# Kernel tuning notes

Hardware: AMD Instinct MI355X
Metric: run time of the kernel (lower is better)

The kernel has to match this reference:

```python
import jax, jax.numpy as jnp
import numpy as np

DIM = 1024
NUM_HEADS = 16
HEAD_DIM = DIM // NUM_HEADS


def setup_inputs() -> dict:
    key = jax.random.key(0)
    ks = jax.random.split(key, 9)
    s = 1.0 / np.sqrt(DIM)
    x = jax.random.normal(ks[0], (2, 2048, DIM), dtype=jnp.float32)
    Wq = jax.random.uniform(ks[1], (DIM, DIM), jnp.float32, -s, s)
    bq = jax.random.uniform(ks[2], (DIM,), jnp.float32, -s, s)
    Wk = jax.random.uniform(ks[3], (DIM, DIM), jnp.float32, -s, s)
    bk = jax.random.uniform(ks[4], (DIM,), jnp.float32, -s, s)
    Wv = jax.random.uniform(ks[5], (DIM, DIM), jnp.float32, -s, s)
    bv = jax.random.uniform(ks[6], (DIM,), jnp.float32, -s, s)
    Wo = jax.random.uniform(ks[7], (DIM, DIM), jnp.float32, -s, s)
    bo = jax.random.uniform(ks[8], (DIM,), jnp.float32, -s, s)
    return {"x": x, "Wq": Wq, "bq": bq, "Wk": Wk, "bk": bk,
            "Wv": Wv, "bv": bv, "Wo": Wo, "bo": bo}


def reference(x, Wq, bq, Wk, bk, Wv, bv, Wo, bo):
    B, S, _ = x.shape
    # projections (torch Linear: y = x @ W.T + b); split heads -> [B, H, S, Dh]
    def split(y):
        return y.reshape(B, S, NUM_HEADS, HEAD_DIM).transpose(0, 2, 1, 3)
    q = split(x @ Wq.T + bq)
    k = split(x @ Wk.T + bk)
    v = split(x @ Wv.T + bv)
    scale = 1.0 / np.sqrt(HEAD_DIM).astype(np.float32)
    scores = jnp.einsum('bhqd,bhkd->bhqk', q, k) * scale  # [B,H,S,S]
    attn = jax.nn.softmax(scores, axis=-1)
    ctx = jnp.einsum('bhqk,bhkd->bhqd', attn, v)  # [B,H,S,Dh]
    ctx = ctx.transpose(0, 2, 1, 3).reshape(B, S, DIM)
    return ctx @ Wo.T + bo
```

## Files before the change

kernel.cpp:

```cpp
#include <hip/hip_runtime.h>
#include <hip/hip_bf16.h>
#include <math.h>

#define DIMSZ 1024
#define NHEAD 16
#define HDIM 64
#define BATCH 2
#define SEQ 2048
#define NROWS (BATCH * SEQ)

#define QSCALE 0.18033688011112042592f

typedef __attribute__((ext_vector_type(8))) _Float16 f16x8;
typedef __attribute__((ext_vector_type(2))) __fp16 fp16x2;
typedef __attribute__((ext_vector_type(4))) float f32x4;

__device__ __forceinline__ ushort f2h(float x) {
    union { _Float16 h; ushort u; } cv;
    cv.h = (_Float16)x;
    return cv.u;
}

__device__ __forceinline__ unsigned pkrtz(float a, float b) {
    union { fp16x2 v; unsigned u; } c;
    c.v = __builtin_amdgcn_cvt_pkrtz(a, b);
    return c.u;
}

__device__ __forceinline__ void gld16(const void* g, void* l) {
    __builtin_amdgcn_global_load_lds((const __attribute__((address_space(1))) void*)g,
                                     (__attribute__((address_space(3))) void*)l,
                                     16, 0, 0);
}

__global__ __launch_bounds__(256) void convert_all(
    const float* __restrict__ x,
    const float* __restrict__ Wq, const float* __restrict__ Wk,
    const float* __restrict__ Wv, const float* __restrict__ Wo,
    ushort* __restrict__ Xh, ushort* __restrict__ Wh, ushort* __restrict__ Woh)
{
    const int b = blockIdx.x;
    const float* src;
    ushort* dst;
    size_t off;
    if (b < 2048)      { src = x;  dst = Xh;             off = (size_t)b * 2048; }
    else if (b < 2560) { src = Wq; dst = Wh;             off = (size_t)(b - 2048) * 2048; }
    else if (b < 3072) { src = Wk; dst = Wh + (1 << 20); off = (size_t)(b - 2560) * 2048; }
    else if (b < 3584) { src = Wv; dst = Wh + 2 * (1 << 20); off = (size_t)(b - 3072) * 2048; }
    else               { src = Wo; dst = Woh;            off = (size_t)(b - 3584) * 2048; }

    const size_t i = off + (size_t)threadIdx.x * 8;
    const float4 f0 = *(const float4*)&src[i];
    const float4 f1 = *(const float4*)&src[i + 4];
    uint4 hv;
    hv.x = (unsigned)f2h(f0.x) | ((unsigned)f2h(f0.y) << 16);
    hv.y = (unsigned)f2h(f0.z) | ((unsigned)f2h(f0.w) << 16);
    hv.z = (unsigned)f2h(f1.x) | ((unsigned)f2h(f1.y) << 16);
    hv.w = (unsigned)f2h(f1.z) | ((unsigned)f2h(f1.w) << 16);
    *(uint4*)&dst[i] = hv;
}

__global__ __launch_bounds__(256, 3) void qkv_gemm(
    const ushort* __restrict__ Xh,
    const ushort* __restrict__ Wh,
    const float* __restrict__ bq, const float* __restrict__ bk,
    const float* __restrict__ bv,
    ushort* __restrict__ Qb, ushort* __restrict__ Kb, ushort* __restrict__ Vt)
{
    __shared__ __align__(16) ushort smem[17408];

    const int tid = threadIdx.x;
    const int wave = tid >> 6;
    const int lane = tid & 63;
    const int lm = lane & 15;
    const int lq = lane >> 4;
    const int wy = wave >> 1;
    const int wx = wave & 1;
    const int m0 = blockIdx.x * 128;
    const int nbase = blockIdx.y * 128;

    const int c = tid & 7;
    const int r0 = tid >> 3;
    const int g = c ^ (r0 & 7);
    const ushort* gah = Xh + (size_t)(m0 + r0) * DIMSZ + g * 8;
    const ushort* gbh = Wh + (size_t)(nbase + r0) * DIMSZ + g * 8;
    const int tofs = tid * 8;

    int aofs[4][2], bofs[4][2];
#pragma unroll
    for (int i = 0; i < 4; ++i)
#pragma unroll
        for (int kt = 0; kt < 2; ++kt) {
            const int slot = ((kt * 4 + lq) ^ (lm & 7)) << 3;
            aofs[i][kt] = (wy * 64 + i * 16 + lm) * 64 + slot;
            bofs[i][kt] = 8192 + (wx * 64 + i * 16 + lm) * 64 + slot;
        }

    f32x4 acc[4][4] = {};

#pragma unroll
    for (int gg = 0; gg < 4; ++gg) {
        gld16(gah + gg * 32 * DIMSZ, smem + gg * 2048 + tofs);
        gld16(gbh + gg * 32 * DIMSZ, smem + 8192 + gg * 2048 + tofs);
    }

    for (int kk = 0; kk < 16; ++kk) {
        __syncthreads();

        f16x8 a0[4], b0[4];
#pragma unroll
        for (int i = 0; i < 4; ++i) {
            a0[i] = *(const f16x8*)&smem[aofs[i][0]];
            b0[i] = *(const f16x8*)&smem[bofs[i][0]];
        }
#pragma unroll
        for (int i = 0; i < 4; ++i)
#pragma unroll
            for (int j = 0; j < 4; ++j)
                acc[i][j] = __builtin_amdgcn_mfma_f32_16x16x32_f16(a0[i], b0[j], acc[i][j], 0, 0, 0);

        f16x8 a1[4], b1[4];
#pragma unroll
        for (int i = 0; i < 4; ++i) {
            a1[i] = *(const f16x8*)&smem[aofs[i][1]];
            b1[i] = *(const f16x8*)&smem[bofs[i][1]];
        }

        __syncthreads();

        if (kk + 1 < 16) {
            const int k0 = (kk + 1) * 64;
#pragma unroll
            for (int gg = 0; gg < 4; ++gg) {
                gld16(gah + gg * 32 * DIMSZ + k0, smem + gg * 2048 + tofs);
                gld16(gbh + gg * 32 * DIMSZ + k0, smem + 8192 + gg * 2048 + tofs);
            }
        }

#pragma unroll
        for (int i = 0; i < 4; ++i)
#pragma unroll
            for (int j = 0; j < 4; ++j)
                acc[i][j] = __builtin_amdgcn_mfma_f32_16x16x32_f16(a1[i], b1[j], acc[i][j], 0, 0, 0);
    }

    const int mat = blockIdx.y >> 3;
    const float* bias = (mat == 0) ? bq : (mat == 1) ? bk : bv;
    const int nloc0 = (blockIdx.y & 7) * 128;
    const int b = m0 >> 11;
    const int s0 = m0 & (SEQ - 1);
    ushort* sf = smem;

    __syncthreads();

    if (mat == 2) {
#pragma unroll
        for (int j = 0; j < 4; ++j) {
            const int nc = nloc0 + wx * 64 + j * 16 + lm;
            const float bb = bias[nc];
            const int d = j * 16 + lm;
#pragma unroll
            for (int i = 0; i < 4; ++i) {
                const int ss = wy * 64 + (i >> 1) * 32 + lq * 8 + (i & 1) * 4;
                ushort4 pk;
                pk.x = f2h(acc[i][j][0] + bb);
                pk.y = f2h(acc[i][j][1] + bb);
                pk.z = f2h(acc[i][j][2] + bb);
                pk.w = f2h(acc[i][j][3] + bb);
                *(ushort4*)&sf[(wx * 64 + d) * 136 + ss] = pk;
            }
        }
        __syncthreads();
#pragma unroll
        for (int p = 0; p < 8; ++p) {
            const int idx = p * 256 + tid;
            const int row = idx >> 4;
            const int hh = row >> 6;
            const int d = row & 63;
            const int sseg = (idx & 15) * 8;
            const uint4 v = *(const uint4*)&sf[row * 136 + sseg];
            const int hg = (nloc0 >> 6) + hh;
            *(uint4*)&Vt[((size_t)(b * NHEAD + hg) * HDIM + d) * SEQ + s0 + sseg] = v;
        }
    } else {
        ushort* dst = (mat == 0) ? Qb : Kb;
        const float sc = (mat == 0) ? QSCALE : 1.0f;
#pragma unroll
        for (int j = 0; j < 4; ++j) {
            const int col = wx * 64 + j * 16 + lm;
            const float bb = bias[nloc0 + col];
#pragma unroll
            for (int i = 0; i < 4; ++i) {
                const int rbase = wy * 64 + i * 16 + lq * 4;
#pragma unroll
                for (int rr = 0; rr < 4; ++rr)
                    sf[(rbase + rr) * 136 + col] = f2h((acc[i][j][rr] + bb) * sc);
            }
        }
        __syncthreads();
#pragma unroll
        for (int p = 0; p < 8; ++p) {
            const int idx = p * 256 + tid;
            const int row = idx >> 4;
            const int seg = idx & 15;
            const uint4 v = *(const uint4*)&sf[row * 136 + seg * 8];
            const int nc0 = nloc0 + seg * 8;
            const int h = nc0 >> 6;
            const int d = nc0 & 63;
            *(uint4*)&dst[((size_t)(b * NHEAD + h) * SEQ + s0 + row) * HDIM + d] = v;
        }
    }
}

__global__ __launch_bounds__(256, 2) void flash_attn_mfma(
    const ushort* __restrict__ Qb, const ushort* __restrict__ Kb,
    const ushort* __restrict__ Vt, ushort* __restrict__ CTXh)
{
    __shared__ __align__(16) ushort Ks[2][8192];
    __shared__ __align__(16) ushort Vs[2][8192];

    const int tid = threadIdx.x;
    const int w = tid >> 6;
    const int l = tid & 63;
    const int lm = l & 15;
    const int lq = l >> 4;
    const int q0 = blockIdx.x * 128;
    const int bh = blockIdx.y;
    const int NCH = SEQ / 128;

    const int ch0 = (bh >> 4) * 8;

    const ushort* Kg = Kb + (size_t)bh * SEQ * HDIM;
    const ushort* Vg = Vt + (size_t)bh * HDIM * SEQ;

    const int sr8 = l >> 3;
    const int sg_ = (l & 7) ^ (sr8 & 7);

    f16x8 qf[2][2];
#pragma unroll
    for (int rt = 0; rt < 2; ++rt)
#pragma unroll
        for (int kt = 0; kt < 2; ++kt)
            qf[rt][kt] = *(const f16x8*)&Qb[((size_t)bh * SEQ + q0 + w * 32 + rt * 16 + lm) * HDIM + kt * 32 + lq * 8];

    int kbase[2], vbase[4];
#pragma unroll
    for (int kt = 0; kt < 2; ++kt)
        kbase[kt] = lm * 64 + (((kt * 4 + lq) ^ (lm & 7)) << 3);
#pragma unroll
    for (int kt2 = 0; kt2 < 4; ++kt2)
        vbase[kt2] = (kt2 >> 1) * 4096 + lm * 64 + ((((kt2 & 1) * 4 + lq) ^ (lm & 7)) << 3);

    f16x8 vones;
#pragma unroll
    for (int i = 0; i < 8; ++i) vones[i] = (_Float16)1.0f;

    f32x4 o[2][4] = {};
    f32x4 lacc[2] = {};

    {
        const int kc0 = ch0 * 128;
#pragma unroll
        for (int p = 0; p < 2; ++p) {
            const int kr = kc0 + p * 64 + w * 16 + sr8;
            gld16(Kg + (size_t)kr * HDIM + sg_ * 8,        &Ks[0][0] + p * 4096 + w * 1024);
            gld16(Kg + (size_t)(kr + 8) * HDIM + sg_ * 8,  &Ks[0][0] + p * 4096 + w * 1024 + 512);
            const int vr = w * 16 + sr8;
            gld16(Vg + (size_t)vr * SEQ + kc0 + p * 64 + sg_ * 8,       &Vs[0][0] + p * 4096 + w * 1024);
            gld16(Vg + (size_t)(vr + 8) * SEQ + kc0 + p * 64 + sg_ * 8, &Vs[0][0] + p * 4096 + w * 1024 + 512);
        }
    }

    for (int it = 0; it < NCH; ++it) {
        __syncthreads();

        if (it + 1 < NCH) {
            const int kc = ((ch0 + it + 1) & (NCH - 1)) * 128;
            ushort* kb_n = &Ks[(it + 1) & 1][0];
            ushort* vb_n = &Vs[(it + 1) & 1][0];
#pragma unroll
            for (int p = 0; p < 2; ++p) {
                const int kr = kc + p * 64 + w * 16 + sr8;
                gld16(Kg + (size_t)kr * HDIM + sg_ * 8,        kb_n + p * 4096 + w * 1024);
                gld16(Kg + (size_t)(kr + 8) * HDIM + sg_ * 8,  kb_n + p * 4096 + w * 1024 + 512);
                const int vr = w * 16 + sr8;
                gld16(Vg + (size_t)vr * SEQ + kc + p * 64 + sg_ * 8,       vb_n + p * 4096 + w * 1024);
                gld16(Vg + (size_t)(vr + 8) * SEQ + kc + p * 64 + sg_ * 8, vb_n + p * 4096 + w * 1024 + 512);
            }
        }

        const ushort* kb = &Ks[it & 1][0];
        const ushort* vb = &Vs[it & 1][0];

        f32x4 st[2][8] = {};
        __builtin_amdgcn_s_setprio(1);
#pragma unroll
        for (int ct = 0; ct < 8; ++ct)
#pragma unroll
            for (int kt = 0; kt < 2; ++kt) {
                const f16x8 kf = *(const f16x8*)&kb[ct * 1024 + kbase[kt]];
                st[0][ct] = __builtin_amdgcn_mfma_f32_16x16x32_f16(kf, qf[0][kt], st[0][ct], 0, 0, 0);
                st[1][ct] = __builtin_amdgcn_mfma_f32_16x16x32_f16(kf, qf[1][kt], st[1][ct], 0, 0, 0);
            }
        __builtin_amdgcn_s_setprio(0);

#pragma unroll
        for (int rt = 0; rt < 2; ++rt)
#pragma unroll
            for (int ct = 0; ct < 8; ++ct)
#pragma unroll
                for (int r = 0; r < 4; ++r)
                    st[rt][ct][r] = __builtin_amdgcn_exp2f(st[rt][ct][r]);

        f16x8 pf[2][4];
#pragma unroll
        for (int rt = 0; rt < 2; ++rt)
#pragma unroll
            for (int kt2 = 0; kt2 < 4; ++kt2) {
                union { f16x8 v; unsigned u[4]; } pk;
#pragma unroll
                for (int t = 0; t < 2; ++t) {
                    pk.u[t * 2 + 0] = pkrtz(st[rt][kt2 * 2 + t][0], st[rt][kt2 * 2 + t][1]);
                    pk.u[t * 2 + 1] = pkrtz(st[rt][kt2 * 2 + t][2], st[rt][kt2 * 2 + t][3]);
                }
                pf[rt][kt2] = pk.v;
            }

        __builtin_amdgcn_s_setprio(1);
#pragma unroll
        for (int kt2 = 0; kt2 < 4; ++kt2) {
            lacc[0] = __builtin_amdgcn_mfma_f32_16x16x32_f16(pf[0][kt2], vones, lacc[0], 0, 0, 0);
            lacc[1] = __builtin_amdgcn_mfma_f32_16x16x32_f16(pf[1][kt2], vones, lacc[1], 0, 0, 0);
        }

#pragma unroll
        for (int dt = 0; dt < 4; ++dt)
#pragma unroll
            for (int kt2 = 0; kt2 < 4; ++kt2) {
                const f16x8 vf = *(const f16x8*)&vb[dt * 1024 + vbase[kt2]];
                o[0][dt] = __builtin_amdgcn_mfma_f32_16x16x32_f16(pf[0][kt2], vf, o[0][dt], 0, 0, 0);
                o[1][dt] = __builtin_amdgcn_mfma_f32_16x16x32_f16(pf[1][kt2], vf, o[1][dt], 0, 0, 0);
            }
        __builtin_amdgcn_s_setprio(0);
    }

    const int b = bh >> 4;
    const int h = bh & 15;
#pragma unroll
    for (int rt = 0; rt < 2; ++rt)
#pragma unroll
    for (int r = 0; r < 4; ++r) {
        const float lr = 1.0f / lacc[rt][r];
        const int srow2 = q0 + w * 32 + rt * 16 + lq * 4 + r;
        const size_t base = ((size_t)b * SEQ + srow2) * DIMSZ + h * HDIM;
#pragma unroll
        for (int dt = 0; dt < 4; ++dt)
            CTXh[base + dt * 16 + lm] = f2h(o[rt][dt][r] * lr);
    }
}

__global__ __launch_bounds__(256) void oproj_gemm(
    const ushort* __restrict__ Ah_g, const ushort* __restrict__ Bh_g,
    const float* __restrict__ bias, float* __restrict__ out)
{
    __shared__ __align__(16) ushort smem[12288];

    const int tid = threadIdx.x;
    const int wave = tid >> 6;
    const int lane = tid & 63;
    const int lm = lane & 15;
    const int lq = lane >> 4;
    const int wy = wave >> 1;
    const int wx = wave & 1;
    const int m0 = blockIdx.x * 64;
    const int n0 = blockIdx.y * 128;

    const int c = tid & 7;
    const int r0 = tid >> 3;
    const int g = c ^ (r0 & 7);
    const ushort* gah = Ah_g + (size_t)(m0 + r0) * DIMSZ + g * 8;
    const ushort* gbh = Bh_g + (size_t)(n0 + r0) * DIMSZ + g * 8;
    const int tofs = tid * 8;

    int aofs[2][2], bofs[4][2];
#pragma unroll
    for (int kt = 0; kt < 2; ++kt) {
        const int slot = ((kt * 4 + lq) ^ (lm & 7)) << 3;
#pragma unroll
        for (int i = 0; i < 2; ++i)
            aofs[i][kt] = (wy * 32 + i * 16 + lm) * 64 + slot;
#pragma unroll
        for (int j = 0; j < 4; ++j)
            bofs[j][kt] = 4096 + (wx * 64 + j * 16 + lm) * 64 + slot;
    }

    f32x4 acc[2][4] = {};

    {
        gld16(gah, smem + tofs);
        gld16(gah + 32 * DIMSZ, smem + 2048 + tofs);
#pragma unroll
        for (int gg = 0; gg < 4; ++gg)
            gld16(gbh + gg * 32 * DIMSZ, smem + 4096 + gg * 2048 + tofs);
    }

    for (int kk = 0; kk < 16; ++kk) {
        __syncthreads();

        f16x8 a0[2], b0[4];
#pragma unroll
        for (int i = 0; i < 2; ++i) a0[i] = *(const f16x8*)&smem[aofs[i][0]];
#pragma unroll
        for (int j = 0; j < 4; ++j) b0[j] = *(const f16x8*)&smem[bofs[j][0]];
#pragma unroll
        for (int i = 0; i < 2; ++i)
#pragma unroll
            for (int j = 0; j < 4; ++j)
                acc[i][j] = __builtin_amdgcn_mfma_f32_16x16x32_f16(a0[i], b0[j], acc[i][j], 0, 0, 0);

        f16x8 a1[2], b1[4];
#pragma unroll
        for (int i = 0; i < 2; ++i) a1[i] = *(const f16x8*)&smem[aofs[i][1]];
#pragma unroll
        for (int j = 0; j < 4; ++j) b1[j] = *(const f16x8*)&smem[bofs[j][1]];

        __syncthreads();

        if (kk + 1 < 16) {
            const int k0 = (kk + 1) * 64;
            gld16(gah + k0, smem + tofs);
            gld16(gah + 32 * DIMSZ + k0, smem + 2048 + tofs);
#pragma unroll
            for (int gg = 0; gg < 4; ++gg)
                gld16(gbh + gg * 32 * DIMSZ + k0, smem + 4096 + gg * 2048 + tofs);
        }

#pragma unroll
        for (int i = 0; i < 2; ++i)
#pragma unroll
            for (int j = 0; j < 4; ++j)
                acc[i][j] = __builtin_amdgcn_mfma_f32_16x16x32_f16(a1[i], b1[j], acc[i][j], 0, 0, 0);
    }

#pragma unroll
    for (int j = 0; j < 4; ++j) {
        const int nc = n0 + wx * 64 + j * 16 + lm;
        const float bb = bias[nc];
#pragma unroll
        for (int i = 0; i < 2; ++i) {
            const int mb = m0 + wy * 32 + i * 16 + lq * 4;
#pragma unroll
            for (int rr = 0; rr < 4; ++rr)
                out[(size_t)(mb + rr) * DIMSZ + nc] = acc[i][j][rr] + bb;
        }
    }
}

extern "C" void kernel_launch(void* const* d_in, const int* in_sizes, int n_in,
                              void* d_out, int out_size, void* d_ws, size_t ws_size,
                              hipStream_t stream)
{
    const float* x  = (const float*)d_in[0];
    const float* Wq = (const float*)d_in[1];
    const float* bq = (const float*)d_in[2];
    const float* Wk = (const float*)d_in[3];
    const float* bk = (const float*)d_in[4];
    const float* Wv = (const float*)d_in[5];
    const float* bv = (const float*)d_in[6];
    const float* Wo = (const float*)d_in[7];
    const float* bo = (const float*)d_in[8];
    float* out = (float*)d_out;

    const size_t elems = (size_t)NROWS * DIMSZ;
    ushort* Qb   = (ushort*)d_ws;
    ushort* Kb   = Qb + elems;
    ushort* Vt   = Kb + elems;
    ushort* CTXh = Vt + elems;
    ushort* Wh   = CTXh + elems;
    ushort* Woh  = Wh + 3 * (1 << 20);
    ushort* Xh   = CTXh;

    convert_all<<<4096, 256, 0, stream>>>(x, Wq, Wk, Wv, Wo, Xh, Wh, Woh);

    qkv_gemm<<<dim3(32, 24), 256, 0, stream>>>(Xh, Wh, bq, bk, bv, Qb, Kb, Vt);

    flash_attn_mfma<<<dim3(SEQ / 128, BATCH * NHEAD), 256, 0, stream>>>(Qb, Kb, Vt, CTXh);

    oproj_gemm<<<dim3(64, 8), 256, 0, stream>>>(CTXh, Woh, bo, out);
}
```

Baseline: 175.3 us.

## Double-buffer LDS in QKV and output-projection GEMMs with staggered K start

Both GEMM kernels now keep two LDS stage buffers, issuing the next K-tile's global-to-LDS loads at the top of each iteration so they overlap the current tile's MFMA work, and dropping the second barrier per iteration. Odd blocks also begin the K loop halfway through and wrap around, spreading concurrent reads of the same weight columns. The price is doubled shared memory per block, and the occupancy hint of 3 blocks per CU is removed from the QKV kernel, which can reduce resident blocks.

```diff
diff --git a/kernel.cpp b/kernel.cpp
--- a/kernel.cpp
+++ b/kernel.cpp
@@ -60,14 +60,14 @@
     *(uint4*)&dst[i] = hv;
 }
 
-__global__ __launch_bounds__(256, 3) void qkv_gemm(
+__global__ __launch_bounds__(256) void qkv_gemm(
     const ushort* __restrict__ Xh,
     const ushort* __restrict__ Wh,
     const float* __restrict__ bq, const float* __restrict__ bk,
     const float* __restrict__ bv,
     ushort* __restrict__ Qb, ushort* __restrict__ Kb, ushort* __restrict__ Vt)
 {
-    __shared__ __align__(16) ushort smem[17408];
+    __shared__ __align__(16) ushort smem[32768];
 
     const int tid = threadIdx.x;
     const int wave = tid >> 6;
@@ -86,6 +86,8 @@
     const ushort* gbh = Wh + (size_t)(nbase + r0) * DIMSZ + g * 8;
     const int tofs = tid * 8;
 
+    const int kk0 = (blockIdx.x & 1) * 8;
+
     int aofs[4][2], bofs[4][2];
 #pragma unroll
     for (int i = 0; i < 4; ++i)
@@ -98,20 +100,35 @@
 
     f32x4 acc[4][4] = {};
 
-#pragma unroll
-    for (int gg = 0; gg < 4; ++gg) {
-        gld16(gah + gg * 32 * DIMSZ, smem + gg * 2048 + tofs);
-        gld16(gbh + gg * 32 * DIMSZ, smem + 8192 + gg * 2048 + tofs);
-    }
-
-    for (int kk = 0; kk < 16; ++kk) {
+    {
+        const int k0 = kk0 * 64;
+#pragma unroll
+        for (int gg = 0; gg < 4; ++gg) {
+            gld16(gah + gg * 32 * DIMSZ + k0, smem + gg * 2048 + tofs);
+            gld16(gbh + gg * 32 * DIMSZ + k0, smem + 8192 + gg * 2048 + tofs);
+        }
+    }
+
+    for (int it = 0; it < 16; ++it) {
         __syncthreads();
 
+        if (it + 1 < 16) {
+            const int k0 = ((kk0 + it + 1) & 15) * 64;
+            ushort* nb = smem + ((it + 1) & 1) * 16384;
+#pragma unroll
+            for (int gg = 0; gg < 4; ++gg) {
+                gld16(gah + gg * 32 * DIMSZ + k0, nb + gg * 2048 + tofs);
+                gld16(gbh + gg * 32 * DIMSZ + k0, nb + 8192 + gg * 2048 + tofs);
+            }
+        }
+
+        const ushort* cb = smem + (it & 1) * 16384;
+
         f16x8 a0[4], b0[4];
 #pragma unroll
         for (int i = 0; i < 4; ++i) {
-            a0[i] = *(const f16x8*)&smem[aofs[i][0]];
-            b0[i] = *(const f16x8*)&smem[bofs[i][0]];
+            a0[i] = *(const f16x8*)&cb[aofs[i][0]];
+            b0[i] = *(const f16x8*)&cb[bofs[i][0]];
         }
 #pragma unroll
         for (int i = 0; i < 4; ++i)
@@ -122,21 +139,9 @@
         f16x8 a1[4], b1[4];
 #pragma unroll
         for (int i = 0; i < 4; ++i) {
-            a1[i] = *(const f16x8*)&smem[aofs[i][1]];
-            b1[i] = *(const f16x8*)&smem[bofs[i][1]];
-        }
-
-        __syncthreads();
-
-        if (kk + 1 < 16) {
-            const int k0 = (kk + 1) * 64;
-#pragma unroll
-            for (int gg = 0; gg < 4; ++gg) {
-                gld16(gah + gg * 32 * DIMSZ + k0, smem + gg * 2048 + tofs);
-                gld16(gbh + gg * 32 * DIMSZ + k0, smem + 8192 + gg * 2048 + tofs);
-            }
-        }
-
+            a1[i] = *(const f16x8*)&cb[aofs[i][1]];
+            b1[i] = *(const f16x8*)&cb[bofs[i][1]];
+        }
 #pragma unroll
         for (int i = 0; i < 4; ++i)
 #pragma unroll
@@ -363,7 +368,7 @@
     const ushort* __restrict__ Ah_g, const ushort* __restrict__ Bh_g,
     const float* __restrict__ bias, float* __restrict__ out)
 {
-    __shared__ __align__(16) ushort smem[12288];
+    __shared__ __align__(16) ushort smem[24576];
 
     const int tid = threadIdx.x;
     const int wave = tid >> 6;
@@ -382,6 +387,8 @@
     const ushort* gbh = Bh_g + (size_t)(n0 + r0) * DIMSZ + g * 8;
     const int tofs = tid * 8;
 
+    const int kk0 = (blockIdx.x & 1) * 8;
+
     int aofs[2][2], bofs[4][2];
 #pragma unroll
     for (int kt = 0; kt < 2; ++kt) {
@@ -397,21 +404,34 @@
     f32x4 acc[2][4] = {};
 
     {
-        gld16(gah, smem + tofs);
-        gld16(gah + 32 * DIMSZ, smem + 2048 + tofs);
+        const int k0 = kk0 * 64;
+        gld16(gah + k0, smem + tofs);
+        gld16(gah + 32 * DIMSZ + k0, smem + 2048 + tofs);
 #pragma unroll
         for (int gg = 0; gg < 4; ++gg)
-            gld16(gbh + gg * 32 * DIMSZ, smem + 4096 + gg * 2048 + tofs);
-    }
-
-    for (int kk = 0; kk < 16; ++kk) {
+            gld16(gbh + gg * 32 * DIMSZ + k0, smem + 4096 + gg * 2048 + tofs);
+    }
+
+    for (int it = 0; it < 16; ++it) {
         __syncthreads();
 
+        if (it + 1 < 16) {
+            const int k0 = ((kk0 + it + 1) & 15) * 64;
+            ushort* nb = smem + ((it + 1) & 1) * 12288;
+            gld16(gah + k0, nb + tofs);
+            gld16(gah + 32 * DIMSZ + k0, nb + 2048 + tofs);
+#pragma unroll
+            for (int gg = 0; gg < 4; ++gg)
+                gld16(gbh + gg * 32 * DIMSZ + k0, nb + 4096 + gg * 2048 + tofs);
+        }
+
+        const ushort* cb = smem + (it & 1) * 12288;
+
         f16x8 a0[2], b0[4];
 #pragma unroll
-        for (int i = 0; i < 2; ++i) a0[i] = *(const f16x8*)&smem[aofs[i][0]];
-#pragma unroll
-        for (int j = 0; j < 4; ++j) b0[j] = *(const f16x8*)&smem[bofs[j][0]];
+        for (int i = 0; i < 2; ++i) a0[i] = *(const f16x8*)&cb[aofs[i][0]];
+#pragma unroll
+        for (int j = 0; j < 4; ++j) b0[j] = *(const f16x8*)&cb[bofs[j][0]];
 #pragma unroll
         for (int i = 0; i < 2; ++i)
 #pragma unroll
@@ -420,21 +440,9 @@
 
         f16x8 a1[2], b1[4];
 #pragma unroll
-        for (int i = 0; i < 2; ++i) a1[i] = *(const f16x8*)&smem[aofs[i][1]];
-#pragma unroll
-        for (int j = 0; j < 4; ++j) b1[j] = *(const f16x8*)&smem[bofs[j][1]];
-
-        __syncthreads();
-
-        if (kk + 1 < 16) {
-            const int k0 = (kk + 1) * 64;
-            gld16(gah + k0, smem + tofs);
-            gld16(gah + 32 * DIMSZ + k0, smem + 2048 + tofs);
-#pragma unroll
-            for (int gg = 0; gg < 4; ++gg)
-                gld16(gbh + gg * 32 * DIMSZ + k0, smem + 4096 + gg * 2048 + tofs);
-        }
-
+        for (int i = 0; i < 2; ++i) a1[i] = *(const f16x8*)&cb[aofs[i][1]];
+#pragma unroll
+        for (int j = 0; j < 4; ++j) b1[j] = *(const f16x8*)&cb[bofs[j][1]];
 #pragma unroll
         for (int i = 0; i < 2; ++i)
 #pragma unroll
```

Measured after the change: 180.2 us. 2.8% more time.
